# Optimization experiments

Measured on AMD Instinct MI355X. Metric: run time of the kernel, lower is better.

Reference implementation:

```python
import jax, jax.numpy as jnp
import numpy as np

INF = 1000000000000.0
B, H, EMB = 64, 512, 512
V = 32000
S_ENC, S_SEQ = 512, 512
ENC2 = 512  # 2 * encoder_hidden_dim
NUM_OOV = 50


def setup_inputs() -> dict:
    key = jax.random.key(0)
    ks = jax.random.split(key, 24)
    s = 0.02
    nrm = lambda k, shp: jax.random.normal(k, shp, jnp.float32) * s
    inp = {}
    inp["input_ids"] = jax.random.randint(ks[0], (B,), 0, V)
    inp["prev_context"] = jax.random.normal(ks[1], (B, H), jnp.float32)
    inp["h0"] = jax.random.normal(ks[2], (1, B, H), jnp.float32)
    inp["c0"] = jax.random.normal(ks[3], (1, B, H), jnp.float32)
    inp["encoder_outputs"] = jax.random.normal(ks[4], (B, S_ENC, H), jnp.float32)
    inp["seqs_encoding"] = jax.random.normal(ks[5], (B, S_SEQ, ENC2), jnp.float32)
    inp["seqs_encoding_mask"] = jax.random.randint(ks[6], (B, S_SEQ), 0, 2).astype(bool)
    ext = jax.random.randint(ks[7], (B, S_SEQ), 0, V + NUM_OOV)
    inp["ext_idx"] = ext.at[0, 0].set(V + NUM_OOV - 1)  # pin max so num_oov=NUM_OOV
    # parameters (torch Linear convention: y = x @ W.T + b)
    inp["embed"] = nrm(ks[8], (V, EMB))
    inp["W_reduce"] = nrm(ks[9], (EMB, EMB + H)); inp["b_reduce"] = jnp.zeros((EMB,), jnp.float32)
    inp["W_key"] = nrm(ks[10], (H, H)); inp["b_key"] = jnp.zeros((H,), jnp.float32)
    inp["W_comb"] = nrm(ks[11], (H, 2 * H)); inp["b_comb"] = jnp.zeros((H,), jnp.float32)
    inp["W_seqkey"] = nrm(ks[12], (H, ENC2))
    inp["W_ih"] = nrm(ks[13], (4 * H, EMB)); inp["W_hh"] = nrm(ks[14], (4 * H, H))
    inp["b_ih"] = jnp.zeros((4 * H,), jnp.float32); inp["b_hh"] = jnp.zeros((4 * H,), jnp.float32)
    inp["W_out"] = nrm(ks[15], (V, H)); inp["b_out"] = jnp.zeros((V,), jnp.float32)
    return inp


def reference(input_ids, prev_context, h0, c0, encoder_outputs, seqs_encoding,
              seqs_encoding_mask, ext_idx, embed, W_reduce, b_reduce, W_key, b_key,
              W_comb, b_comb, W_seqkey, W_ih, W_hh, b_ih, b_hh, W_out, b_out):
    # embed + (dropout is identity at p=0 / eval) + reduce
    embedded = embed[input_ids]                                   # [B, EMB]
    x = jnp.concatenate([embedded, prev_context], axis=1) @ W_reduce.T + b_reduce  # [B, EMB]
    # single-step, single-layer LSTM (PyTorch gate order i, f, g, o)
    h, c = h0[0], c0[0]
    gates = x @ W_ih.T + b_ih + h @ W_hh.T + b_hh                 # [B, 4H]
    i, f, g, o = jnp.split(gates, 4, axis=-1)
    c1 = jax.nn.sigmoid(f) * c + jax.nn.sigmoid(i) * jnp.tanh(g)
    h1 = jax.nn.sigmoid(o) * jnp.tanh(c1)                         # [B, H]
    output = h1
    # masked attention over encoder_outputs
    enc_mask = encoder_outputs.sum(axis=-1) == 0                  # [B, S_enc]
    keys = encoder_outputs @ W_key.T + b_key                      # [B, S_enc, H]
    energies = jnp.einsum('bsh,bh->bs', keys, output)
    energies = jnp.where(enc_mask, 1e-12, energies)
    attn_weights = jax.nn.softmax(energies, axis=-1)
    context = jnp.einsum('bs,bsh->bh', attn_weights, encoder_outputs)  # [B, H]
    combined = jnp.tanh(jnp.concatenate([output, context], axis=1) @ W_comb.T + b_comb)
    logits = combined @ W_out.T + b_out                           # [B, V]
    # masked attention energies over token sequence for the copy mechanism
    seq_keys = jnp.tanh(seqs_encoding @ W_seqkey.T)               # [B, S_seq, H]
    seq_energies = jnp.einsum('bsh,bh->bs', seq_keys, output)
    seq_energies = jnp.where(seqs_encoding_mask, 1e-12, seq_energies)
    # extended vocab + scatter_max pointer-copy
    extended = jnp.concatenate([logits, jnp.zeros((B, NUM_OOV), logits.dtype)], axis=1)  # [B, V+OOV]
    copy = jnp.full_like(extended, -INF)
    copy = copy.at[jnp.arange(B)[:, None], ext_idx].max(seq_energies)
    copy = jnp.where(copy == -INF, 0.0, copy)
    out = extended + copy
    out = jnp.where(out == 0.0, -INF, out)
    out = jax.nn.log_softmax(out, axis=1)
    return (out, context, h1[None], c1[None], attn_weights)
```

## Files before the change

kernel.cpp:

```cpp
#include <hip/hip_runtime.h>
#include <math.h>

#define B_N    64
#define H_N    512
#define V_N    32000
#define S_N    512
#define VEXT   32050
#define INF_F  1000000000000.0f

typedef __attribute__((ext_vector_type(4))) float floatx4;
typedef __attribute__((ext_vector_type(8))) __bf16 bf16x8;

#define OFF_OUT0 0
#define OFF_CTX  (B_N * VEXT)
#define OFF_H1   (OFF_CTX + B_N * H_N)
#define OFF_C1   (OFF_H1 + B_N * H_N)
#define OFF_ATTN (OFF_C1 + B_N * H_N)

#define WS_FLAG   0
#define WS_X      16
#define WS_GATES  (WS_X + B_N * H_N)
#define WS_Q      (WS_GATES + B_N * 4 * H_N)
#define WS_KB     (WS_Q + B_N * H_N)
#define WS_EN     (WS_KB + B_N)
#define WS_COMB   (WS_EN + B_N * S_N)
#define WS_SEQE   (WS_COMB + B_N * H_N)
#define WS_WSKBF  (WS_SEQE + B_N * S_N)
#define WS_LOGITS (WS_WSKBF + (H_N * H_N) / 2)
#define WS_COPY   (WS_LOGITS + B_N * V_N)

__device__ __forceinline__ float sigm(float x) { return 1.0f / (1.0f + expf(-x)); }

__device__ __forceinline__ unsigned short f2bf(float f) {
    unsigned u = __float_as_uint(f);
    u += 0x7fffu + ((u >> 16) & 1u);
    return (unsigned short)(u >> 16);
}

__device__ __forceinline__ unsigned enc_f(float f) {
    unsigned u = __float_as_uint(f);
    return (u & 0x80000000u) ? ~u : (u | 0x80000000u);
}
__device__ __forceinline__ float dec_f(unsigned e) {
    unsigned u = (e & 0x80000000u) ? (e & 0x7fffffffu) : ~e;
    return __uint_as_float(u);
}

__global__ void kDetect(const unsigned int* __restrict__ m, int* __restrict__ flag) {
    __shared__ int any;
    if (threadIdx.x == 0) any = 0;
    __syncthreads();
    int loc = 0;
    for (int i = threadIdx.x; i < 8192; i += 256) loc |= (m[i] > 1u) ? 1 : 0;
    if (loc) any = 1;
    __syncthreads();
    if (threadIdx.x == 0) *flag = any;
}

__global__ void kConvertW(const float* __restrict__ W, unsigned short* __restrict__ wsk) {
    const int i = (blockIdx.x * 256 + threadIdx.x) * 4;
    float4 v = *(const float4*)(W + i);
    ushort4 h;
    h.x = f2bf(v.x); h.y = f2bf(v.y); h.z = f2bf(v.z); h.w = f2bf(v.w);
    *(ushort4*)(wsk + i) = h;
}

__global__ void kFillCopy(unsigned int* __restrict__ copyenc) {
    const unsigned NE = enc_f(-INF_F);
    int i0 = (blockIdx.x * 256 + threadIdx.x) * 4;
#pragma unroll
    for (int k = 0; k < 4; k++) {
        int i = i0 + k;
        if (i < B_N * VEXT) copyenc[i] = NE;
    }
}

__global__ __launch_bounds__(256) void kEmbedReduce(
        const int* __restrict__ ids, const float* __restrict__ embed,
        const float* __restrict__ pctx, const float* __restrict__ Wred,
        const float* __restrict__ bred, float* __restrict__ x) {
    __shared__ float xc[1024];
    const int tid = threadIdx.x;
    const int b = blockIdx.x >> 1, half = blockIdx.x & 1;
    const float* er = embed + (size_t)ids[b] * 512;
    xc[tid] = er[tid];               xc[tid + 256] = er[tid + 256];
    xc[512 + tid] = pctx[b * 512 + tid]; xc[512 + tid + 256] = pctx[b * 512 + tid + 256];
    __syncthreads();
    const int j = half * 256 + tid;
    const float4* w4 = (const float4*)(Wred + (size_t)j * 1024);
    const float4* x4 = (const float4*)xc;
    float acc = bred[j];
    for (int k = 0; k < 256; k++) {
        float4 w = w4[k], xv = x4[k];
        acc += w.x * xv.x + w.y * xv.y + w.z * xv.z + w.w * xv.w;
    }
    x[b * 512 + j] = acc;
}

__global__ __launch_bounds__(256) void kGates(
        const float* __restrict__ x, const float* __restrict__ h0,
        const float* __restrict__ Wih, const float* __restrict__ Whh,
        const float* __restrict__ bih, const float* __restrict__ bhh,
        float* __restrict__ gates) {
    __shared__ float xl[512], hl[512];
    const int tid = threadIdx.x;
    const int b = blockIdx.x >> 3, part = blockIdx.x & 7;
    xl[tid] = x[b * 512 + tid];  xl[tid + 256] = x[b * 512 + tid + 256];
    hl[tid] = h0[b * 512 + tid]; hl[tid + 256] = h0[b * 512 + tid + 256];
    __syncthreads();
    const int j = part * 256 + tid;
    const float4* wi4 = (const float4*)(Wih + (size_t)j * 512);
    const float4* wh4 = (const float4*)(Whh + (size_t)j * 512);
    const float4* x4 = (const float4*)xl;
    const float4* h4 = (const float4*)hl;
    float acc = bih[j] + bhh[j];
    for (int k = 0; k < 128; k++) {
        float4 w = wi4[k], xv = x4[k];
        acc += w.x * xv.x + w.y * xv.y + w.z * xv.z + w.w * xv.w;
    }
    for (int k = 0; k < 128; k++) {
        float4 w = wh4[k], hv = h4[k];
        acc += w.x * hv.x + w.y * hv.y + w.z * hv.z + w.w * hv.w;
    }
    gates[(size_t)b * 2048 + j] = acc;
}

__global__ __launch_bounds__(256) void kLstm(
        const float* __restrict__ gates, const float* __restrict__ c0,
        float* __restrict__ h1o, float* __restrict__ c1o) {
    const int idx = blockIdx.x * 256 + threadIdx.x;
    const int b = idx >> 9, j = idx & 511;
    const float gi = gates[(size_t)b * 2048 + j];
    const float gf = gates[(size_t)b * 2048 + 512 + j];
    const float gg = gates[(size_t)b * 2048 + 1024 + j];
    const float go = gates[(size_t)b * 2048 + 1536 + j];
    const float cp = c0[idx];
    const float c1 = sigm(gf) * cp + sigm(gi) * tanhf(gg);
    const float h1 = sigm(go) * tanhf(c1);
    h1o[idx] = h1;
    c1o[idx] = c1;
}

__global__ __launch_bounds__(256) void kQ(
        const float* __restrict__ h1, const float* __restrict__ Wkey,
        const float* __restrict__ bkey, float* __restrict__ q, float* __restrict__ kb) {
    __shared__ float hl[512];
    __shared__ float rd[256];
    const int tid = threadIdx.x;
    const int b = blockIdx.x >> 1, half = blockIdx.x & 1;
    hl[tid] = h1[b * 512 + tid]; hl[tid + 256] = h1[b * 512 + tid + 256];
    __syncthreads();
    const int k = half * 256 + tid;
    float acc = 0.f;
#pragma unroll 4
    for (int h = 0; h < 512; h++) acc += hl[h] * Wkey[(size_t)h * 512 + k];
    q[b * 512 + k] = acc;
    if (half == 0) {
        float p = bkey[tid] * hl[tid] + bkey[tid + 256] * hl[tid + 256];
        rd[tid] = p; __syncthreads();
        for (int st = 128; st > 0; st >>= 1) {
            if (tid < st) rd[tid] += rd[tid + st];
            __syncthreads();
        }
        if (tid == 0) kb[b] = rd[0];
    }
}

__global__ __launch_bounds__(256) void kEnergies(
        const float* __restrict__ enc, const float* __restrict__ q,
        const float* __restrict__ kb, float* __restrict__ energ) {
    __shared__ float ql[512];
    __shared__ float pe[256], ps[256];
    const int tid = threadIdx.x;
    const int b = blockIdx.x >> 2;
    const int sc = (blockIdx.x & 3) * 128;
    ql[tid] = q[b * 512 + tid]; ql[tid + 256] = q[b * 512 + tid + 256];
    __syncthreads();
    const int r = tid & 127, hi = tid >> 7;
    const float4* row4 = (const float4*)(enc + (size_t)(b * 512 + sc + r) * 512 + hi * 256);
    const float4* q4 = (const float4*)(ql + hi * 256);
    float e = 0.f, ssum = 0.f;
#pragma unroll 4
    for (int k = 0; k < 64; k++) {
        float4 ev = row4[k], qv = q4[k];
        e += ev.x * qv.x + ev.y * qv.y + ev.z * qv.z + ev.w * qv.w;
        ssum += ev.x + ev.y + ev.z + ev.w;
    }
    pe[tid] = e; ps[tid] = ssum;
    __syncthreads();
    if (tid < 128) {
        float ee = pe[tid] + pe[tid + 128] + kb[b];
        float sm = ps[tid] + ps[tid + 128];
        if (sm == 0.0f) ee = 1e-12f;
        energ[b * 512 + sc + tid] = ee;
    }
}

__global__ __launch_bounds__(256) void kSoftmax(
        const float* __restrict__ energ, float* __restrict__ attn) {
    __shared__ float el[512];
    __shared__ float rd[256];
    const int tid = threadIdx.x, b = blockIdx.x;
    el[tid] = energ[b * 512 + tid]; el[tid + 256] = energ[b * 512 + tid + 256];
    __syncthreads();
    rd[tid] = fmaxf(el[tid], el[tid + 256]); __syncthreads();
    for (int st = 128; st > 0; st >>= 1) {
        if (tid < st) rd[tid] = fmaxf(rd[tid], rd[tid + st]);
        __syncthreads();
    }
    const float m = rd[0]; __syncthreads();
    float v0 = expf(el[tid] - m), v1 = expf(el[tid + 256] - m);
    rd[tid] = v0 + v1; __syncthreads();
    for (int st = 128; st > 0; st >>= 1) {
        if (tid < st) rd[tid] += rd[tid + st];
        __syncthreads();
    }
    const float inv = 1.0f / rd[0];
    attn[b * 512 + tid] = v0 * inv;
    attn[b * 512 + tid + 256] = v1 * inv;
}

__global__ __launch_bounds__(256) void kContext(
        const float* __restrict__ enc, const float* __restrict__ attn,
        float* __restrict__ ctx) {
    __shared__ float al[64];
    const int tid = threadIdx.x;
    const int b = blockIdx.x >> 3, sc = (blockIdx.x & 7) * 64;
    if (tid < 64) al[tid] = attn[b * 512 + sc + tid];
    __syncthreads();
    float a0 = 0.f, a1 = 0.f;
    for (int s = 0; s < 64; s++) {
        const float* row = enc + (size_t)(b * 512 + sc + s) * 512;
        const float av = al[s];
        a0 += av * row[tid];
        a1 += av * row[tid + 256];
    }
    atomicAdd(&ctx[b * 512 + tid], a0);
    atomicAdd(&ctx[b * 512 + tid + 256], a1);
}

__global__ __launch_bounds__(256) void kCombined(
        const float* __restrict__ h1, const float* __restrict__ ctx,
        const float* __restrict__ Wcomb, const float* __restrict__ bcomb,
        float* __restrict__ comb) {
    __shared__ float hc[1024];
    const int tid = threadIdx.x;
    const int b = blockIdx.x >> 1, half = blockIdx.x & 1;
    hc[tid] = h1[b * 512 + tid];        hc[tid + 256] = h1[b * 512 + tid + 256];
    hc[512 + tid] = ctx[b * 512 + tid]; hc[512 + tid + 256] = ctx[b * 512 + tid + 256];
    __syncthreads();
    const int j = half * 256 + tid;
    const float4* w4 = (const float4*)(Wcomb + (size_t)j * 1024);
    const float4* x4 = (const float4*)hc;
    float acc = bcomb[j];
    for (int k = 0; k < 256; k++) {
        float4 w = w4[k], xv = x4[k];
        acc += w.x * xv.x + w.y * xv.y + w.z * xv.z + w.w * xv.w;
    }
    comb[b * 512 + j] = tanhf(acc);
}

__global__ __launch_bounds__(256) void kLogits(
        const float* __restrict__ comb, const float* __restrict__ Wout,
        const float* __restrict__ bout, float* __restrict__ logits) {
    __shared__ float cl[4][32][64];
    const int tid = threadIdx.x;
    const int vt = tid & 63, kq = tid >> 6;
    const int v = blockIdx.x * 64 + vt;
    float acc[64];
#pragma unroll
    for (int i = 0; i < 64; i++) acc[i] = 0.f;
    for (int kc = 0; kc < 4; kc++) {
        __syncthreads();
        {
            const float4* s4 = (const float4*)(comb + (size_t)vt * 512 + kq * 128 + kc * 32);
#pragma unroll
            for (int qq = 0; qq < 8; qq++) {
                float4 vv = s4[qq];
                cl[kq][qq * 4 + 0][vt] = vv.x; cl[kq][qq * 4 + 1][vt] = vv.y;
                cl[kq][qq * 4 + 2][vt] = vv.z; cl[kq][qq * 4 + 3][vt] = vv.w;
            }
        }
        __syncthreads();
        float wreg[32];
        const float4* w4 = (const float4*)(Wout + (size_t)v * 512 + kq * 128 + kc * 32);
#pragma unroll
        for (int qq = 0; qq < 8; qq++) {
            float4 wv = w4[qq];
            wreg[qq * 4 + 0] = wv.x; wreg[qq * 4 + 1] = wv.y;
            wreg[qq * 4 + 2] = wv.z; wreg[qq * 4 + 3] = wv.w;
        }
#pragma unroll
        for (int kk = 0; kk < 32; kk++) {
            const float wv = wreg[kk];
            const float4* cp = (const float4*)&cl[kq][kk][0];
#pragma unroll
            for (int b4 = 0; b4 < 16; b4++) {
                float4 c4 = cp[b4];
                acc[b4 * 4 + 0] += wv * c4.x; acc[b4 * 4 + 1] += wv * c4.y;
                acc[b4 * 4 + 2] += wv * c4.z; acc[b4 * 4 + 3] += wv * c4.w;
            }
        }
    }
    float* red = &cl[0][0][0];
    __syncthreads();
    if (kq >= 2) {
#pragma unroll
        for (int b = 0; b < 64; b++) red[(kq - 2) * 4096 + vt * 64 + b] = acc[b];
    }
    __syncthreads();
    if (kq < 2) {
#pragma unroll
        for (int b = 0; b < 64; b++) acc[b] += red[kq * 4096 + vt * 64 + b];
    }
    __syncthreads();
    if (kq == 1) {
#pragma unroll
        for (int b = 0; b < 64; b++) red[vt * 64 + b] = acc[b];
    }
    __syncthreads();
    if (kq == 0) {
        const float bo = bout[v];
#pragma unroll
        for (int b = 0; b < 64; b++)
            logits[(size_t)b * 32000 + v] = acc[b] + red[vt * 64 + b] + bo;
    }
}

__global__ __launch_bounds__(512) void kSeqGemm(
        const float* __restrict__ seqs, const unsigned short* __restrict__ wsk,
        const float* __restrict__ h1g, float* __restrict__ seq_e) {
    __shared__ unsigned short a_lds[64 * 40];
    __shared__ unsigned short b_lds[512 * 40];
    __shared__ float h1l[512];
    __shared__ float partf[8][64];
    const int tid = threadIdx.x;
    const int m0 = blockIdx.x * 64;
    const int b = m0 >> 9;
    const int w = tid >> 6;
    const int lane = tid & 63;
    const int quad = lane >> 4;
    const int c16 = lane & 15;

    h1l[tid] = h1g[b * 512 + tid];

    floatx4 acc[4][4];
    const floatx4 zf = {0.f, 0.f, 0.f, 0.f};
#pragma unroll
    for (int i = 0; i < 4; i++)
#pragma unroll
        for (int j = 0; j < 4; j++) acc[i][j] = zf;

    const int arow = tid >> 3, aseg = tid & 7;
    for (int kc = 0; kc < 16; kc++) {
        const int k0 = kc * 32;
        __syncthreads();
        {
            const float4 v = *(const float4*)(seqs + (size_t)(m0 + arow) * 512 + k0 + aseg * 4);
            ushort4 hv;
            hv.x = f2bf(v.x); hv.y = f2bf(v.y); hv.z = f2bf(v.z); hv.w = f2bf(v.w);
            *(ushort4*)&a_lds[arow * 40 + aseg * 4] = hv;
        }
        {
            const uint4* sp = (const uint4*)(wsk + (size_t)tid * 512 + k0);
            uint4* dp = (uint4*)&b_lds[tid * 40];
            dp[0] = sp[0]; dp[1] = sp[1]; dp[2] = sp[2]; dp[3] = sp[3];
        }
        __syncthreads();
        bf16x8 af[4], bfr[4];
#pragma unroll
        for (int ms = 0; ms < 4; ms++)
            af[ms] = *(const bf16x8*)&a_lds[(ms * 16 + c16) * 40 + quad * 8];
#pragma unroll
        for (int nt = 0; nt < 4; nt++)
            bfr[nt] = *(const bf16x8*)&b_lds[(w * 64 + nt * 16 + c16) * 40 + quad * 8];
#pragma unroll
        for (int ms = 0; ms < 4; ms++)
#pragma unroll
            for (int nt = 0; nt < 4; nt++)
                acc[ms][nt] = __builtin_amdgcn_mfma_f32_16x16x32_bf16(
                    af[ms], bfr[nt], acc[ms][nt], 0, 0, 0);
    }
    float psum[16];
#pragma unroll
    for (int i = 0; i < 16; i++) psum[i] = 0.f;
#pragma unroll
    for (int ms = 0; ms < 4; ms++)
#pragma unroll
        for (int nt = 0; nt < 4; nt++) {
            const float hv = h1l[w * 64 + nt * 16 + c16];
#pragma unroll
            for (int r = 0; r < 4; r++)
                psum[ms * 4 + r] += tanhf(acc[ms][nt][r]) * hv;
        }
#pragma unroll
    for (int d = 1; d < 16; d <<= 1)
#pragma unroll
        for (int i = 0; i < 16; i++) psum[i] += __shfl_xor(psum[i], d);
    if (c16 == 0) {
#pragma unroll
        for (int ms = 0; ms < 4; ms++)
#pragma unroll
            for (int r = 0; r < 4; r++)
                partf[w][ms * 16 + quad * 4 + r] = psum[ms * 4 + r];
    }
    __syncthreads();
    if (tid < 64) {
        float s = 0.f;
#pragma unroll
        for (int ww = 0; ww < 8; ww++) s += partf[ww][tid];
        seq_e[m0 + tid] = s;
    }
}

__global__ __launch_bounds__(512) void kScatter(
        const float* __restrict__ seq_e, const void* __restrict__ mask,
        const int* __restrict__ extix, const int* __restrict__ flag,
        unsigned int* __restrict__ copyenc) {
    const int tid = threadIdx.x, b = blockIdx.x;
    float e = seq_e[b * 512 + tid];
    bool mk;
    if (*flag) mk = ((const unsigned char*)mask)[b * 512 + tid] != 0;
    else       mk = ((const int*)mask)[b * 512 + tid] != 0;
    if (mk) e = 1e-12f;
    const int idx = extix[b * 512 + tid];
    atomicMax(&copyenc[(size_t)b * VEXT + idx], enc_f(e));
}

__global__ __launch_bounds__(256) void kFinal(
        const float* __restrict__ logits, const unsigned int* __restrict__ copyenc,
        float* __restrict__ out0) {
    __shared__ float rd[256];
    const int tid = threadIdx.x, b = blockIdx.x;
    const float* lrow = logits + (size_t)b * 32000;
    const unsigned int* crow = copyenc + (size_t)b * VEXT;
    float* orow = out0 + (size_t)b * VEXT;
    float lm = -3.0e38f;
    for (int j = tid; j < VEXT; j += 256) {
        float ext = (j < 32000) ? lrow[j] : 0.0f;
        float cv = dec_f(crow[j]);
        if (cv == -INF_F) cv = 0.0f;
        float o = ext + cv;
        if (o == 0.0f) o = -INF_F;
        orow[j] = o;
        lm = fmaxf(lm, o);
    }
    rd[tid] = lm; __syncthreads();
    for (int st = 128; st > 0; st >>= 1) {
        if (tid < st) rd[tid] = fmaxf(rd[tid], rd[tid + st]);
        __syncthreads();
    }
    const float m = rd[0]; __syncthreads();
    float ls = 0.f;
    for (int j = tid; j < VEXT; j += 256) ls += expf(orow[j] - m);
    rd[tid] = ls; __syncthreads();
    for (int st = 128; st > 0; st >>= 1) {
        if (tid < st) rd[tid] += rd[tid + st];
        __syncthreads();
    }
    const float lse = m + logf(rd[0]);
    __syncthreads();
    for (int j = tid; j < VEXT; j += 256) orow[j] -= lse;
}

extern "C" void kernel_launch(void* const* d_in, const int* in_sizes, int n_in,
                              void* d_out, int out_size, void* d_ws, size_t ws_size,
                              hipStream_t stream) {
    const int*   ids   = (const int*)d_in[0];
    const float* pctx  = (const float*)d_in[1];
    const float* h0    = (const float*)d_in[2];
    const float* c0    = (const float*)d_in[3];
    const float* enc   = (const float*)d_in[4];
    const float* seqs  = (const float*)d_in[5];
    const void*  mask  = d_in[6];
    const int*   extix = (const int*)d_in[7];
    const float* embed = (const float*)d_in[8];
    const float* Wred  = (const float*)d_in[9];
    const float* bred  = (const float*)d_in[10];
    const float* Wkey  = (const float*)d_in[11];
    const float* bkey  = (const float*)d_in[12];
    const float* Wcomb = (const float*)d_in[13];
    const float* bcomb = (const float*)d_in[14];
    const float* Wseqk = (const float*)d_in[15];
    const float* Wih   = (const float*)d_in[16];
    const float* Whh   = (const float*)d_in[17];
    const float* bih   = (const float*)d_in[18];
    const float* bhh   = (const float*)d_in[19];
    const float* Wout  = (const float*)d_in[20];
    const float* bout  = (const float*)d_in[21];
    (void)in_sizes; (void)n_in; (void)out_size; (void)ws_size;

    float* out = (float*)d_out;
    float* ws = (float*)d_ws;
    int* flag = (int*)ws;
    float* xws = ws + WS_X;
    float* gatesws = ws + WS_GATES;
    float* qws = ws + WS_Q;
    float* kbws = ws + WS_KB;
    float* enws = ws + WS_EN;
    float* combws = ws + WS_COMB;
    float* seqews = ws + WS_SEQE;
    unsigned short* wsk = (unsigned short*)(ws + WS_WSKBF);
    float* logitsws = ws + WS_LOGITS;
    unsigned int* copyenc = (unsigned int*)(ws + WS_COPY);

    kDetect<<<1, 256, 0, stream>>>((const unsigned int*)mask, flag);
    kConvertW<<<256, 256, 0, stream>>>(Wseqk, wsk);
    kFillCopy<<<2004, 256, 0, stream>>>(copyenc);
    kEmbedReduce<<<128, 256, 0, stream>>>(ids, embed, pctx, Wred, bred, xws);
    kGates<<<512, 256, 0, stream>>>(xws, h0, Wih, Whh, bih, bhh, gatesws);
    kLstm<<<128, 256, 0, stream>>>(gatesws, c0, out + OFF_H1, out + OFF_C1);
    kQ<<<128, 256, 0, stream>>>(out + OFF_H1, Wkey, bkey, qws, kbws);
    kEnergies<<<256, 256, 0, stream>>>(enc, qws, kbws, enws);
    kSoftmax<<<64, 256, 0, stream>>>(enws, out + OFF_ATTN);
    hipMemsetAsync(out + OFF_CTX, 0, (size_t)B_N * H_N * sizeof(float), stream);
    kContext<<<512, 256, 0, stream>>>(enc, out + OFF_ATTN, out + OFF_CTX);
    kCombined<<<128, 256, 0, stream>>>(out + OFF_H1, out + OFF_CTX, Wcomb, bcomb, combws);
    kLogits<<<500, 256, 0, stream>>>(combws, Wout, bout, logitsws);
    kSeqGemm<<<512, 512, 0, stream>>>(seqs, wsk, out + OFF_H1, seqews);
    kScatter<<<64, 512, 0, stream>>>(seqews, mask, extix, flag, copyenc);
    kFinal<<<64, 256, 0, stream>>>(logitsws, copyenc, out + OFF_OUT0);
}
```

Before: 685.8 us.

## Split final log-softmax into three grid-wide kernels with atomic row reductions

Measured after the change: 607.2 us. -11.5%, faster.

```diff
diff --git a/kernel.cpp b/kernel.cpp
--- a/kernel.cpp
+++ b/kernel.cpp
@@ -28,6 +28,8 @@
 #define WS_WSKBF  (WS_SEQE + B_N * S_N)
 #define WS_LOGITS (WS_WSKBF + (H_N * H_N) / 2)
 #define WS_COPY   (WS_LOGITS + B_N * V_N)
+#define WS_RMAX   (WS_COPY + B_N * VEXT)
+#define WS_RSUM   (WS_RMAX + B_N)
 
 __device__ __forceinline__ float sigm(float x) { return 1.0f / (1.0f + expf(-x)); }
 
@@ -65,8 +67,13 @@
     *(ushort4*)(wsk + i) = h;
 }
 
-__global__ void kFillCopy(unsigned int* __restrict__ copyenc) {
+__global__ void kFillCopy(unsigned int* __restrict__ copyenc,
+                          unsigned int* __restrict__ rmax, float* __restrict__ rsum) {
     const unsigned NE = enc_f(-INF_F);
+    if (blockIdx.x == 0 && threadIdx.x < B_N) {
+        rmax[threadIdx.x] = 0u;
+        rsum[threadIdx.x] = 0.0f;
+    }
     int i0 = (blockIdx.x * 256 + threadIdx.x) * 4;
 #pragma unroll
     for (int k = 0; k < 4; k++) {
@@ -427,40 +434,75 @@
     atomicMax(&copyenc[(size_t)b * VEXT + idx], enc_f(e));
 }
 
-__global__ __launch_bounds__(256) void kFinal(
+__global__ __launch_bounds__(256) void kFinal1(
         const float* __restrict__ logits, const unsigned int* __restrict__ copyenc,
-        float* __restrict__ out0) {
-    __shared__ float rd[256];
-    const int tid = threadIdx.x, b = blockIdx.x;
+        float* __restrict__ out0, unsigned int* __restrict__ rmax) {
+    __shared__ float rd[4];
+    const int tid = threadIdx.x;
+    const int b = blockIdx.x >> 4, chunk = blockIdx.x & 15;
+    const int base = chunk * 2048 + tid;
     const float* lrow = logits + (size_t)b * 32000;
     const unsigned int* crow = copyenc + (size_t)b * VEXT;
     float* orow = out0 + (size_t)b * VEXT;
     float lm = -3.0e38f;
-    for (int j = tid; j < VEXT; j += 256) {
-        float ext = (j < 32000) ? lrow[j] : 0.0f;
-        float cv = dec_f(crow[j]);
-        if (cv == -INF_F) cv = 0.0f;
-        float o = ext + cv;
-        if (o == 0.0f) o = -INF_F;
-        orow[j] = o;
-        lm = fmaxf(lm, o);
-    }
-    rd[tid] = lm; __syncthreads();
-    for (int st = 128; st > 0; st >>= 1) {
-        if (tid < st) rd[tid] = fmaxf(rd[tid], rd[tid + st]);
-        __syncthreads();
-    }
-    const float m = rd[0]; __syncthreads();
-    float ls = 0.f;
-    for (int j = tid; j < VEXT; j += 256) ls += expf(orow[j] - m);
-    rd[tid] = ls; __syncthreads();
-    for (int st = 128; st > 0; st >>= 1) {
-        if (tid < st) rd[tid] += rd[tid + st];
-        __syncthreads();
-    }
-    const float lse = m + logf(rd[0]);
-    __syncthreads();
-    for (int j = tid; j < VEXT; j += 256) orow[j] -= lse;
+#pragma unroll
+    for (int k = 0; k < 8; k++) {
+        const int j = base + k * 256;
+        if (j < VEXT) {
+            float ext = (j < 32000) ? lrow[j] : 0.0f;
+            float cv = dec_f(crow[j]);
+            if (cv == -INF_F) cv = 0.0f;
+            float o = ext + cv;
+            if (o == 0.0f) o = -INF_F;
+            orow[j] = o;
+            lm = fmaxf(lm, o);
+        }
+    }
+#pragma unroll
+    for (int d = 1; d < 64; d <<= 1) lm = fmaxf(lm, __shfl_xor(lm, d));
+    if ((tid & 63) == 0) rd[tid >> 6] = lm;
+    __syncthreads();
+    if (tid == 0) {
+        float m = fmaxf(fmaxf(rd[0], rd[1]), fmaxf(rd[2], rd[3]));
+        atomicMax(&rmax[b], enc_f(m));
+    }
+}
+
+__global__ __launch_bounds__(256) void kFinal2(
+        const float* __restrict__ out0, const unsigned int* __restrict__ rmax,
+        float* __restrict__ rsum) {
+    __shared__ float rd[4];
+    const int tid = threadIdx.x;
+    const int b = blockIdx.x >> 4, chunk = blockIdx.x & 15;
+    const int base = chunk * 2048 + tid;
+    const float* orow = out0 + (size_t)b * VEXT;
+    const float m = dec_f(rmax[b]);
+    float s = 0.f;
+#pragma unroll
+    for (int k = 0; k < 8; k++) {
+        const int j = base + k * 256;
+        if (j < VEXT) s += expf(orow[j] - m);
+    }
+#pragma unroll
+    for (int d = 1; d < 64; d <<= 1) s += __shfl_xor(s, d);
+    if ((tid & 63) == 0) rd[tid >> 6] = s;
+    __syncthreads();
+    if (tid == 0) atomicAdd(&rsum[b], rd[0] + rd[1] + rd[2] + rd[3]);
+}
+
+__global__ __launch_bounds__(256) void kFinal3(
+        float* __restrict__ out0, const unsigned int* __restrict__ rmax,
+        const float* __restrict__ rsum) {
+    const int tid = threadIdx.x;
+    const int b = blockIdx.x >> 4, chunk = blockIdx.x & 15;
+    const int base = chunk * 2048 + tid;
+    float* orow = out0 + (size_t)b * VEXT;
+    const float lse = dec_f(rmax[b]) + logf(rsum[b]);
+#pragma unroll
+    for (int k = 0; k < 8; k++) {
+        const int j = base + k * 256;
+        if (j < VEXT) orow[j] -= lse;
+    }
 }
 
 extern "C" void kernel_launch(void* const* d_in, const int* in_sizes, int n_in,
@@ -503,10 +545,12 @@
     unsigned short* wsk = (unsigned short*)(ws + WS_WSKBF);
     float* logitsws = ws + WS_LOGITS;
     unsigned int* copyenc = (unsigned int*)(ws + WS_COPY);
+    unsigned int* rmax = (unsigned int*)(ws + WS_RMAX);
+    float* rsum = ws + WS_RSUM;
 
     kDetect<<<1, 256, 0, stream>>>((const unsigned int*)mask, flag);
     kConvertW<<<256, 256, 0, stream>>>(Wseqk, wsk);
-    kFillCopy<<<2004, 256, 0, stream>>>(copyenc);
+    kFillCopy<<<2004, 256, 0, stream>>>(copyenc, rmax, rsum);
     kEmbedReduce<<<128, 256, 0, stream>>>(ids, embed, pctx, Wred, bred, xws);
     kGates<<<512, 256, 0, stream>>>(xws, h0, Wih, Whh, bih, bhh, gatesws);
     kLstm<<<128, 256, 0, stream>>>(gatesws, c0, out + OFF_H1, out + OFF_C1);
@@ -519,5 +563,7 @@
     kLogits<<<500, 256, 0, stream>>>(combws, Wout, bout, logitsws);
     kSeqGemm<<<512, 512, 0, stream>>>(seqs, wsk, out + OFF_H1, seqews);
     kScatter<<<64, 512, 0, stream>>>(seqews, mask, extix, flag, copyenc);
-    kFinal<<<64, 256, 0, stream>>>(logitsws, copyenc, out + OFF_OUT0);
-}
+    kFinal1<<<1024, 256, 0, stream>>>(logitsws, copyenc, out + OFF_OUT0, rmax);
+    kFinal2<<<1024, 256, 0, stream>>>(out + OFF_OUT0, rmax, rsum);
+    kFinal3<<<1024, 256, 0, stream>>>(out + OFF_OUT0, rmax, rsum);
+}
```
